# Optimization experiments

Measured on AMD Instinct MI355X. Metric: run time of the kernel, lower is better.

## Reference

```python
import jax, jax.numpy as jnp
import numpy as np
from jax import lax


def conv2d(x, w, pad):
    # NCHW / OIHW, stride 1, symmetric padding
    return lax.conv_general_dilated(x, w, (1, 1), [(pad, pad), (pad, pad)],
                                    dimension_numbers=('NCHW', 'OIHW', 'NCHW'))


def maxpool2(x):
    return lax.reduce_window(x, -jnp.inf, lax.max, (1, 1, 2, 2), (1, 1, 2, 2), 'VALID')


def batchnorm(x, g, b, eps=1e-5):
    # training-mode BN: batch statistics over (N,H,W), biased variance (matches torch)
    m = x.mean(axis=(0, 2, 3), keepdims=True)
    v = x.var(axis=(0, 2, 3), keepdims=True)
    return (x - m) * lax.rsqrt(v + eps) * g[None, :, None, None] + b[None, :, None, None]


def setup_inputs() -> dict:
    key = jax.random.key(0)
    ks = jax.random.split(key, 10)
    rn = lambda k, shape, s=0.1: jax.random.normal(k, shape, jnp.float32) * s
    return {
        'X': jax.random.normal(ks[0], (32, 3, 128, 128), jnp.float32),
        'obs': jax.random.normal(ks[1], (32, 4), jnp.float32),
        'h1_w': rn(ks[2], (64, 3, 3, 3)), 'h1_b': jnp.zeros((64,), jnp.float32),
        'bn1_g': jnp.ones((64,), jnp.float32), 'bn1_b': jnp.zeros((64,), jnp.float32),
        'h2_w': rn(ks[3], (128, 64, 3, 3)), 'h2_b': jnp.zeros((128,), jnp.float32),
        'bn2_g': jnp.ones((128,), jnp.float32), 'bn2_b': jnp.zeros((128,), jnp.float32),
        'h3_w': rn(ks[4], (128, 128, 3, 3)), 'h3_b': jnp.zeros((128,), jnp.float32),
        'bn3_g': jnp.ones((128,), jnp.float32), 'bn3_b': jnp.zeros((128,), jnp.float32),
        'r_w': rn(ks[5], (1, 128, 1, 1)),
        'q_w': rn(ks[6], (16, 1, 5, 5)),
        'w_vi': rn(ks[7], (16, 1, 5, 5)),
        'crit_w': rn(ks[8], (1, 256)), 'crit_b': jnp.zeros((1,), jnp.float32),
        'K': 40,
    }


def reference(X, obs, h1_w, h1_b, bn1_g, bn1_b, h2_w, h2_b, bn2_g, bn2_b,
              h3_w, h3_b, bn3_g, bn3_b, r_w, q_w, w_vi, crit_w, crit_b, K):
    # CNN feature extractor (obs is unused in the original forward)
    h = jax.nn.relu(batchnorm(maxpool2(conv2d(X, h1_w, 1) + h1_b[None, :, None, None]), bn1_g, bn1_b))
    h = jax.nn.relu(batchnorm(maxpool2(conv2d(h, h2_w, 1) + h2_b[None, :, None, None]), bn2_g, bn2_b))
    h = jax.nn.relu(batchnorm(maxpool2(conv2d(h, h3_w, 1) + h3_b[None, :, None, None]), bn3_g, bn3_b))
    r = conv2d(h, r_w, 0)                 # [B,1,16,16] reward map
    # conv(concat([r,v]), concat([q_w,w_vi], axis=1)) == conv(r,q_w) + conv(v,w_vi);
    # the r-branch is constant across the VI loop, so compute it once.
    conv_r = conv2d(r, q_w, 2)            # [B,l_q,16,16]
    v = conv_r.max(axis=1, keepdims=True)  # initial q = self.q(r)

    def body(i, v):
        q = conv_r + conv2d(v, w_vi, 2)
        return q.max(axis=1, keepdims=True)

    v = lax.fori_loop(0, K - 1, body, v)
    q = conv_r + conv2d(v, w_vi, 2)       # final explicit step
    v = q.max(axis=1, keepdims=True)
    critic = v.reshape(-1, 256) @ crit_w.T + crit_b  # [B,1]
    return critic, q.reshape(-1, 4096)
```

## Files before the change

kernel.cpp:

```cpp
#include <hip/hip_runtime.h>
#include <hip/hip_bf16.h>


using bf16x8 = __attribute__((ext_vector_type(8))) short;
using f32x4  = __attribute__((ext_vector_type(4))) float;

__device__ __forceinline__ unsigned short f2bf(float x) {
    union { float f; unsigned u; } v; v.f = x;
    unsigned r = (v.u + 0x7FFFu + ((v.u >> 16) & 1u)) >> 16;
    return (unsigned short)r;
}
__device__ __forceinline__ float bfhi(unsigned short h) {
    union { unsigned u; float f; } v; v.u = ((unsigned)h) << 16;
    return v.f;
}

template <int CIN>
__global__ __launch_bounds__(256)
void wt_kernel(const float* __restrict__ W, short* __restrict__ Wh,
               short* __restrict__ Wl)
{
    constexpr int TOTAL = 128 * CIN * 9;
    int i = blockIdx.x * 256 + threadIdx.x;
    if (i >= TOTAL) return;
    int ci = i & (CIN - 1);
    int j  = i / CIN;
    int tap = j % 9, co = j / 9;
    float x = W[(co * CIN + ci) * 9 + tap];
    unsigned short h = f2bf(x);
    Wh[i] = (short)h;
    Wl[i] = (short)f2bf(x - bfhi(h));
}

__global__ __launch_bounds__(256)
void conv1_pool_kernel(const float* __restrict__ X, const float* __restrict__ W,
                       const float* __restrict__ Bias, float* __restrict__ out)
{
    const int sp  = blockIdx.x;
    const int n   = blockIdx.y;
    const int ty0 = (sp >> 2) * 16;
    const int tx0 = (sp & 3) * 16;
    const int tid = threadIdx.x;
    const int px = tid & 15, py = tid >> 4;

    __shared__ float s_in[3][34][34];

    const int gy0 = 2 * ty0 - 1, gx0 = 2 * tx0 - 1;
    for (int idx = tid; idx < 3 * 1156; idx += 256) {
        int ci = idx / 1156, rem = idx - ci * 1156;
        int ly = rem / 34, lx = rem - ly * 34;
        int gy = gy0 + ly, gx = gx0 + lx;
        float v = 0.f;
        if ((unsigned)gy < 128u && (unsigned)gx < 128u)
            v = X[((n * 3 + ci) << 14) + (gy << 7) + gx];
        s_in[ci][ly][lx] = v;
    }
    __syncthreads();

    float patch[3][4][4];
    #pragma unroll
    for (int ci = 0; ci < 3; ++ci)
        #pragma unroll
        for (int r = 0; r < 4; ++r) {
            float2 a = *(const float2*)&s_in[ci][2 * py + r][2 * px];
            float2 b = *(const float2*)&s_in[ci][2 * py + r][2 * px + 2];
            patch[ci][r][0] = a.x; patch[ci][r][1] = a.y;
            patch[ci][r][2] = b.x; patch[ci][r][3] = b.y;
        }

    float* obase = out + (((size_t)(n * 64 + ty0 + py) * 64) + tx0 + px) * 64;
    #pragma unroll 1
    for (int co0 = 0; co0 < 64; co0 += 4) {
        float4 res;
        #pragma unroll
        for (int j = 0; j < 4; ++j) {
            int co = co0 + j;
            float wk[27];
            const float* wp = W + co * 27;
            #pragma unroll
            for (int k = 0; k < 27; ++k) wk[k] = wp[k];
            float b0 = Bias[co];
            float a0 = b0, a1 = b0, a2 = b0, a3 = b0;
            #pragma unroll
            for (int ci = 0; ci < 3; ++ci)
                #pragma unroll
                for (int dy = 0; dy < 3; ++dy)
                    #pragma unroll
                    for (int dx = 0; dx < 3; ++dx) {
                        float w = wk[ci * 9 + dy * 3 + dx];
                        a0 = fmaf(w, patch[ci][dy][dx],     a0);
                        a1 = fmaf(w, patch[ci][dy][dx + 1], a1);
                        a2 = fmaf(w, patch[ci][dy + 1][dx], a2);
                        a3 = fmaf(w, patch[ci][dy + 1][dx + 1], a3);
                    }
            float m = fmaxf(fmaxf(a0, a1), fmaxf(a2, a3));
            if (j == 0) res.x = m; else if (j == 1) res.y = m;
            else if (j == 2) res.z = m; else res.w = m;
        }
        *(float4*)(obase + co0) = res;
    }
}

template <int C>
__global__ __launch_bounds__(256)
void bn_partial_kernel(const float* __restrict__ data, int total,
                       float* __restrict__ partials)
{
    const int b = blockIdx.x, t = threadIdx.x;
    float s = 0.f, s2 = 0.f;
    for (int i = b * 256 + t; i < total; i += 256 * 256) {
        float v = data[i];
        s += v; s2 += v * v;
    }
    __shared__ float rs[256], rs2[256];
    rs[t] = s; rs2[t] = s2;
    __syncthreads();
    if (t < C) {
        #pragma unroll
        for (int off = C; off < 256; off += C) { s += rs[t + off]; s2 += rs2[t + off]; }
        partials[(b * C + t) * 2]     = s;
        partials[(b * C + t) * 2 + 1] = s2;
    }
}

__global__ __launch_bounds__(128)
void bn_finalize_kernel(const float* __restrict__ partials, int C, float cnt,
                        const float* __restrict__ g, const float* __restrict__ bb,
                        float* __restrict__ a_out, float* __restrict__ c_out)
{
    int t = threadIdx.x;
    if (t >= C) return;
    float s = 0.f, s2 = 0.f;
    for (int i = 0; i < 256; ++i) {
        s  += partials[(i * C + t) * 2];
        s2 += partials[(i * C + t) * 2 + 1];
    }
    float mean = s / cnt;
    float var  = s2 / cnt - mean * mean;
    float a = g[t] * rsqrtf(var + 1e-5f);
    a_out[t] = a;
    c_out[t] = bb[t] - mean * a;
}

template <int CIN, int WIN>
__global__ __launch_bounds__(256, 3)
void conv_mfma_kernel(const float* __restrict__ in, const float* __restrict__ bna,
                      const float* __restrict__ bnc, const short* __restrict__ Wth,
                      const short* __restrict__ Wtl, const float* __restrict__ Bias,
                      float* __restrict__ out)
{
    constexpr int CC    = CIN / 32;
    constexpr int POW   = WIN / 2;
    constexpr int TILES = WIN / 16;
    const int bx  = blockIdx.x;
    const int coh = blockIdx.y;
    const int n   = blockIdx.z;
    const int ty = bx / TILES, tx = bx % TILES;
    const int y0 = ty * 16, x0 = tx * 16;
    const int tid  = threadIdx.x;
    const int w    = tid >> 6;
    const int lane = tid & 63;
    const int lrow = lane & 15;
    const int seg  = lane >> 4;

    __shared__ __align__(16) short sA[2][4][324][8];

    f32x4 acc[4][4];
    #pragma unroll
    for (int mf = 0; mf < 4; ++mf)
        #pragma unroll
        for (int nf = 0; nf < 4; ++nf) acc[mf][nf] = (f32x4){0.f, 0.f, 0.f, 0.f};

    #pragma unroll 1
    for (int c = 0; c < CC; ++c) {
        #pragma unroll
        for (int rep = 0; rep < 6; ++rep) {
            int u = tid + rep * 256;
            if (u < 1296) {
                int slot = u / 324, p = u - slot * 324;
                int hy = p / 18, hx = p - hy * 18;
                int y = y0 - 1 + hy, x = x0 - 1 + hx;
                int cb = c * 32 + slot * 8;
                float4 f0 = make_float4(0.f, 0.f, 0.f, 0.f);
                float4 f1 = make_float4(0.f, 0.f, 0.f, 0.f);
                if ((unsigned)y < (unsigned)WIN && (unsigned)x < (unsigned)WIN) {
                    const float* s = in + (size_t)((n * WIN + y) * WIN + x) * CIN + cb;
                    f0 = *(const float4*)s;
                    f1 = *(const float4*)(s + 4);
                }
                float4 a0 = *(const float4*)(bna + cb);
                float4 a1 = *(const float4*)(bna + cb + 4);
                float4 c0 = *(const float4*)(bnc + cb);
                float4 c1 = *(const float4*)(bnc + cb + 4);
                float e[8] = {
                    fmaxf(fmaf(f0.x, a0.x, c0.x), 0.f),
                    fmaxf(fmaf(f0.y, a0.y, c0.y), 0.f),
                    fmaxf(fmaf(f0.z, a0.z, c0.z), 0.f),
                    fmaxf(fmaf(f0.w, a0.w, c0.w), 0.f),
                    fmaxf(fmaf(f1.x, a1.x, c1.x), 0.f),
                    fmaxf(fmaf(f1.y, a1.y, c1.y), 0.f),
                    fmaxf(fmaf(f1.z, a1.z, c1.z), 0.f),
                    fmaxf(fmaf(f1.w, a1.w, c1.w), 0.f)};
                unsigned hpk[4], lpk[4];
                #pragma unroll
                for (int q = 0; q < 4; ++q) {
                    unsigned short h0 = f2bf(e[2 * q]), h1 = f2bf(e[2 * q + 1]);
                    unsigned short l0 = f2bf(e[2 * q] - bfhi(h0));
                    unsigned short l1 = f2bf(e[2 * q + 1] - bfhi(h1));
                    hpk[q] = (unsigned)h0 | ((unsigned)h1 << 16);
                    lpk[q] = (unsigned)l0 | ((unsigned)l1 << 16);
                }
                *(int4*)&sA[0][slot][p][0] =
                    make_int4((int)hpk[0], (int)hpk[1], (int)hpk[2], (int)hpk[3]);
                *(int4*)&sA[1][slot][p][0] =
                    make_int4((int)lpk[0], (int)lpk[1], (int)lpk[2], (int)lpk[3]);
            }
        }
        __syncthreads();

        const short* baseH = &sA[0][0][0][0];
        const short* baseL = &sA[1][0][0][0];
        #pragma unroll 3
        for (int tap = 0; tap < 9; ++tap) {
            const int dy = tap / 3, dx = tap % 3;
            bf16x8 ah[4], al[4];
            #pragma unroll
            for (int mf = 0; mf < 4; ++mf) {
                int idx = seg * 324 + (w * 4 + mf + dy) * 18 + (lrow + dx);
                ah[mf] = *(const bf16x8*)(baseH + idx * 8);
                al[mf] = *(const bf16x8*)(baseL + idx * 8);
            }
            #pragma unroll
            for (int nf = 0; nf < 4; ++nf) {
                int co = coh * 64 + nf * 16 + lrow;
                const short* wp = Wth + ((size_t)(co * 9 + tap)) * CIN + c * 32 + seg * 8;
                const short* wq = Wtl + ((size_t)(co * 9 + tap)) * CIN + c * 32 + seg * 8;
                bf16x8 bh = *(const bf16x8*)wp;
                bf16x8 bl = *(const bf16x8*)wq;
                #pragma unroll
                for (int mf = 0; mf < 4; ++mf) {
                    acc[mf][nf] = __builtin_amdgcn_mfma_f32_16x16x32_bf16(
                        ah[mf], bh, acc[mf][nf], 0, 0, 0);
                    acc[mf][nf] = __builtin_amdgcn_mfma_f32_16x16x32_bf16(
                        al[mf], bh, acc[mf][nf], 0, 0, 0);
                    acc[mf][nf] = __builtin_amdgcn_mfma_f32_16x16x32_bf16(
                        ah[mf], bl, acc[mf][nf], 0, 0, 0);
                }
            }
        }
        __syncthreads();
    }

    #pragma unroll
    for (int mf = 0; mf < 4; mf += 2) {
        const int ypo = (y0 >> 1) + w * 2 + (mf >> 1);
        const int xp0 = (x0 >> 1) + seg * 2;
        #pragma unroll
        for (int nf = 0; nf < 4; ++nf) {
            int co = coh * 64 + nf * 16 + lrow;
            float bv = Bias[co];
            f32x4 u = acc[mf][nf], v = acc[mf + 1][nf];
            float o0 = fmaxf(fmaxf(u[0], u[1]), fmaxf(v[0], v[1]));
            float o1 = fmaxf(fmaxf(u[2], u[3]), fmaxf(v[2], v[3]));
            float* ob = out + (size_t)((n * POW + ypo) * POW + xp0) * 128 + co;
            ob[0]   = o0 + bv;
            ob[128] = o1 + bv;
        }
    }
}

__global__ __launch_bounds__(256)
void vin_kernel(const float* __restrict__ pool3, const float* __restrict__ bn_a,
                const float* __restrict__ bn_c, const float* __restrict__ r_w,
                const float* __restrict__ q_w, const float* __restrict__ w_vi,
                const float* __restrict__ crit_w, const float* __restrict__ crit_b,
                const int* __restrict__ Kp, float* __restrict__ out_critic,
                float* __restrict__ out_q)
{
    const int n = blockIdx.x;
    const int tid = threadIdx.x;
    const int px = tid & 15, py = tid >> 4;

    __shared__ float s_cr[16][256];
    __shared__ float s_v[20][20];
    __shared__ float s_qw[16][25];
    __shared__ float s_wvi[16][25];
    __shared__ float s_rw[128];
    __shared__ float s_red[256];

    for (int i = tid; i < 400; i += 256) {
        s_qw[i / 25][i % 25]  = q_w[i];
        s_wvi[i / 25][i % 25] = w_vi[i];
        s_v[i / 20][i % 20]   = 0.f;
    }
    if (tid < 128) s_rw[tid] = r_w[tid];
    __syncthreads();

    float r = 0.f;
    const float* p3 = pool3 + ((size_t)n * 256 + tid) * 128;
    #pragma unroll 1
    for (int ci0 = 0; ci0 < 128; ci0 += 4) {
        float4 v4 = *(const float4*)(p3 + ci0);
        float e[4] = {v4.x, v4.y, v4.z, v4.w};
        #pragma unroll
        for (int j = 0; j < 4; ++j) {
            float x = fmaxf(fmaf(e[j], bn_a[ci0 + j], bn_c[ci0 + j]), 0.f);
            r = fmaf(x, s_rw[ci0 + j], r);
        }
    }
    s_v[py + 2][px + 2] = r;
    __syncthreads();

    float cr[16];
    #pragma unroll
    for (int co = 0; co < 16; ++co) cr[co] = 0.f;
    #pragma unroll
    for (int dy = 0; dy < 5; ++dy)
        #pragma unroll
        for (int dx = 0; dx < 5; ++dx) {
            float rv = s_v[py + dy][px + dx];
            #pragma unroll
            for (int co = 0; co < 16; ++co)
                cr[co] = fmaf(s_qw[co][dy * 5 + dx], rv, cr[co]);
        }
    float v = cr[0];
    #pragma unroll
    for (int co = 0; co < 16; ++co) { s_cr[co][tid] = cr[co]; v = fmaxf(v, cr[co]); }
    __syncthreads();
    s_v[py + 2][px + 2] = v;
    __syncthreads();

    const int K = Kp[0];
    float q[16];
    #pragma unroll 1
    for (int it = 0; it < K; ++it) {
        #pragma unroll
        for (int co = 0; co < 16; ++co) q[co] = s_cr[co][tid];
        #pragma unroll
        for (int dy = 0; dy < 5; ++dy)
            #pragma unroll
            for (int dx = 0; dx < 5; ++dx) {
                float vv = s_v[py + dy][px + dx];
                #pragma unroll
                for (int co = 0; co < 16; ++co)
                    q[co] = fmaf(s_wvi[co][dy * 5 + dx], vv, q[co]);
            }
        float nv = q[0];
        #pragma unroll
        for (int co = 1; co < 16; ++co) nv = fmaxf(nv, q[co]);
        __syncthreads();
        s_v[py + 2][px + 2] = nv;
        __syncthreads();
        v = nv;
    }

    #pragma unroll
    for (int co = 0; co < 16; ++co)
        out_q[(size_t)n * 4096 + co * 256 + tid] = q[co];

    s_red[tid] = v * crit_w[tid];
    __syncthreads();
    for (int off = 128; off > 0; off >>= 1) {
        if (tid < off) s_red[tid] += s_red[tid + off];
        __syncthreads();
    }
    if (tid == 0) out_critic[n] = s_red[0] + crit_b[0];
}

extern "C" void kernel_launch(void* const* d_in, const int* in_sizes, int n_in,
                              void* d_out, int out_size, void* d_ws, size_t ws_size,
                              hipStream_t stream)
{
    const float* X      = (const float*)d_in[0];
    const float* h1_w   = (const float*)d_in[2];
    const float* h1_b   = (const float*)d_in[3];
    const float* bn1_g  = (const float*)d_in[4];
    const float* bn1_b  = (const float*)d_in[5];
    const float* h2_w   = (const float*)d_in[6];
    const float* h2_b   = (const float*)d_in[7];
    const float* bn2_g  = (const float*)d_in[8];
    const float* bn2_b  = (const float*)d_in[9];
    const float* h3_w   = (const float*)d_in[10];
    const float* h3_b   = (const float*)d_in[11];
    const float* bn3_g  = (const float*)d_in[12];
    const float* bn3_b  = (const float*)d_in[13];
    const float* r_w    = (const float*)d_in[14];
    const float* q_w    = (const float*)d_in[15];
    const float* w_vi   = (const float*)d_in[16];
    const float* crit_w = (const float*)d_in[17];
    const float* crit_b = (const float*)d_in[18];
    const int*   Kp     = (const int*)d_in[19];

    float* ws    = (float*)d_ws;
    short* W2H   = (short*)(ws);
    short* W2L   = (short*)(ws + 36864);
    short* W3H   = (short*)(ws + 73728);
    short* W3L   = (short*)(ws + 147456);
    float* part  = ws + 221184;
    float* prm   = ws + 286720;
    float* a1 = prm, *c1 = prm + 64, *a2 = prm + 128, *c2 = prm + 256,
         * a3 = prm + 384, *c3 = prm + 512;
    float* buf1  = ws + 287744;
    float* buf2  = ws + 8676352;
    float* pool3 = ws + 287744;

    float* out_critic = (float*)d_out;
    float* out_q      = out_critic + 32;

    wt_kernel<64><<<(128 * 64 * 9 + 255) / 256, 256, 0, stream>>>(h2_w, W2H, W2L);
    wt_kernel<128><<<(128 * 128 * 9 + 255) / 256, 256, 0, stream>>>(h3_w, W3H, W3L);

    conv1_pool_kernel<<<dim3(16, 32), 256, 0, stream>>>(X, h1_w, h1_b, buf1);

    bn_partial_kernel<64><<<256, 256, 0, stream>>>(buf1, 8388608, part);
    bn_finalize_kernel<<<1, 128, 0, stream>>>(part, 64, 131072.f, bn1_g, bn1_b, a1, c1);

    conv_mfma_kernel<64, 64><<<dim3(16, 2, 32), 256, 0, stream>>>(
        buf1, a1, c1, W2H, W2L, h2_b, buf2);

    bn_partial_kernel<128><<<256, 256, 0, stream>>>(buf2, 4194304, part);
    bn_finalize_kernel<<<1, 128, 0, stream>>>(part, 128, 32768.f, bn2_g, bn2_b, a2, c2);

    conv_mfma_kernel<128, 32><<<dim3(4, 2, 32), 256, 0, stream>>>(
        buf2, a2, c2, W3H, W3L, h3_b, pool3);

    bn_partial_kernel<128><<<256, 256, 0, stream>>>(pool3, 1048576, part);
    bn_finalize_kernel<<<1, 128, 0, stream>>>(part, 128, 8192.f, bn3_g, bn3_b, a3, c3);

    vin_kernel<<<32, 256, 0, stream>>>(pool3, a3, c3, r_w, q_w, w_vi,
                                       crit_w, crit_b, Kp, out_critic, out_q);
}
```

Baseline: 507.1 us.

## Prefetch next channel chunk during MFMA compute and relayout conv weights

The conv MFMA kernel now issues global loads for the next 32-channel chunk into registers before computing the current chunk, then converts and writes them to LDS afterwards. The goal is to hide global load latency behind the MFMA work. Weights are pre-permuted into a layout that makes each lane's fragment load contiguous, and BN scale/shift are staged in shared memory. Conv3 also splits output channels over four blocks (NF=2) for more parallelism. The extra prefetch registers lower the occupancy hint from 3 to 2 waves.

```diff
diff --git a/kernel.cpp b/kernel.cpp
--- a/kernel.cpp
+++ b/kernel.cpp
@@ -20,16 +20,20 @@
 void wt_kernel(const float* __restrict__ W, short* __restrict__ Wh,
                short* __restrict__ Wl)
 {
+    constexpr int CC = CIN / 32;
     constexpr int TOTAL = 128 * CIN * 9;
     int i = blockIdx.x * 256 + threadIdx.x;
     if (i >= TOTAL) return;
-    int ci = i & (CIN - 1);
+    int ci = i % CIN;
     int j  = i / CIN;
     int tap = j % 9, co = j / 9;
     float x = W[(co * CIN + ci) * 9 + tap];
+    int c = ci >> 5, seg = (ci >> 3) & 3, e = ci & 7;
+    int cb = co >> 4, lr = co & 15;
+    size_t oi = ((((size_t)(tap * CC + c) * 8 + cb) * 4 + seg) * 16 + lr) * 8 + e;
     unsigned short h = f2bf(x);
-    Wh[i] = (short)h;
-    Wl[i] = (short)f2bf(x - bfhi(h));
+    Wh[oi] = (short)h;
+    Wl[oi] = (short)f2bf(x - bfhi(h));
 }
 
 __global__ __launch_bounds__(256)
@@ -142,8 +146,8 @@
     c_out[t] = bb[t] - mean * a;
 }
 
-template <int CIN, int WIN>
-__global__ __launch_bounds__(256, 3)
+template <int CIN, int WIN, int NF>
+__global__ __launch_bounds__(256, 2)
 void conv_mfma_kernel(const float* __restrict__ in, const float* __restrict__ bna,
                       const float* __restrict__ bnc, const short* __restrict__ Wth,
                       const short* __restrict__ Wtl, const float* __restrict__ Bias,
@@ -158,106 +162,139 @@
     const int ty = bx / TILES, tx = bx % TILES;
     const int y0 = ty * 16, x0 = tx * 16;
     const int tid  = threadIdx.x;
-    const int w    = tid >> 6;
+    const int wv   = tid >> 6;
     const int lane = tid & 63;
     const int lrow = lane & 15;
     const int seg  = lane >> 4;
-
-    __shared__ __align__(16) short sA[2][4][324][8];
-
-    f32x4 acc[4][4];
+    const int cbase = coh * NF;
+
+    __shared__ __align__(16) short sAs[2 * 4 * 324 * 8];
+    __shared__ float sBnA[128], sBnC[128];
+
+    if (tid < CIN) { sBnA[tid] = bna[tid]; sBnC[tid] = bnc[tid]; }
+
+    int offs[6], lds16[6], cia[6];
+    unsigned vmask = 0;
+    #pragma unroll
+    for (int rep = 0; rep < 6; ++rep) {
+        int u = tid + rep * 256;
+        int slot = u / 324, p = u - slot * 324;
+        int hy = p / 18, hx = p - hy * 18;
+        int y = y0 - 1 + hy, x = x0 - 1 + hx;
+        bool act = (u < 1296);
+        bool val = act && ((unsigned)y < (unsigned)WIN) && ((unsigned)x < (unsigned)WIN);
+        offs[rep]  = ((n * WIN + y) * WIN + x) * CIN + slot * 8;
+        lds16[rep] = slot * 324 + p;
+        cia[rep]   = slot * 8;
+        if (val) vmask |= 1u << rep;
+    }
+
+    float4 pa[6], pb[6];
+
+#define ISSUE_LOADS(cc) \
+    _Pragma("unroll") \
+    for (int rep = 0; rep < 6; ++rep) { \
+        float4 z; z.x = 0.f; z.y = 0.f; z.z = 0.f; z.w = 0.f; \
+        pa[rep] = z; pb[rep] = z; \
+        if ((vmask >> rep) & 1u) { \
+            const float* s_ = in + offs[rep] + (cc) * 32; \
+            pa[rep] = *(const float4*)s_; \
+            pb[rep] = *(const float4*)(s_ + 4); \
+        } \
+    }
+
+#define CONVERT_WRITE(cc) \
+    _Pragma("unroll") \
+    for (int rep = 0; rep < 6; ++rep) { \
+        if (rep < 5 || tid < 16) { \
+            const float* ba_ = sBnA + (cc) * 32 + cia[rep]; \
+            const float* bc_ = sBnC + (cc) * 32 + cia[rep]; \
+            float4 a0_ = *(const float4*)ba_, a1_ = *(const float4*)(ba_ + 4); \
+            float4 c0_ = *(const float4*)bc_, c1_ = *(const float4*)(bc_ + 4); \
+            float e_[8] = { \
+                fmaxf(fmaf(pa[rep].x, a0_.x, c0_.x), 0.f), \
+                fmaxf(fmaf(pa[rep].y, a0_.y, c0_.y), 0.f), \
+                fmaxf(fmaf(pa[rep].z, a0_.z, c0_.z), 0.f), \
+                fmaxf(fmaf(pa[rep].w, a0_.w, c0_.w), 0.f), \
+                fmaxf(fmaf(pb[rep].x, a1_.x, c1_.x), 0.f), \
+                fmaxf(fmaf(pb[rep].y, a1_.y, c1_.y), 0.f), \
+                fmaxf(fmaf(pb[rep].z, a1_.z, c1_.z), 0.f), \
+                fmaxf(fmaf(pb[rep].w, a1_.w, c1_.w), 0.f)}; \
+            unsigned hpk_[4], lpk_[4]; \
+            _Pragma("unroll") \
+            for (int q = 0; q < 4; ++q) { \
+                unsigned short h0_ = f2bf(e_[2 * q]), h1_ = f2bf(e_[2 * q + 1]); \
+                unsigned short l0_ = f2bf(e_[2 * q] - bfhi(h0_)); \
+                unsigned short l1_ = f2bf(e_[2 * q + 1] - bfhi(h1_)); \
+                hpk_[q] = (unsigned)h0_ | ((unsigned)h1_ << 16); \
+                lpk_[q] = (unsigned)l0_ | ((unsigned)l1_ << 16); \
+            } \
+            *(int4*)&sAs[lds16[rep] * 8] = \
+                make_int4((int)hpk_[0], (int)hpk_[1], (int)hpk_[2], (int)hpk_[3]); \
+            *(int4*)&sAs[10368 + lds16[rep] * 8] = \
+                make_int4((int)lpk_[0], (int)lpk_[1], (int)lpk_[2], (int)lpk_[3]); \
+        } \
+    }
+
+#define COMPUTE(cc) \
+    { const short* baseH_ = sAs; const short* baseL_ = sAs + 10368; \
+      _Pragma("unroll 3") \
+      for (int tap = 0; tap < 9; ++tap) { \
+          const int dy_ = tap / 3, dx_ = tap % 3; \
+          bf16x8 ah_[4], al_[4]; \
+          _Pragma("unroll") \
+          for (int mf = 0; mf < 4; ++mf) { \
+              int idx_ = seg * 324 + (wv * 4 + mf + dy_) * 18 + (lrow + dx_); \
+              ah_[mf] = *(const bf16x8*)(baseH_ + idx_ * 8); \
+              al_[mf] = *(const bf16x8*)(baseL_ + idx_ * 8); \
+          } \
+          _Pragma("unroll") \
+          for (int nf = 0; nf < NF; ++nf) { \
+              size_t wo_ = ((((size_t)(tap * CC + (cc)) * 8 + cbase + nf) * 4 + seg) * 16 + lrow) * 8; \
+              bf16x8 bh_ = *(const bf16x8*)(Wth + wo_); \
+              bf16x8 bl_ = *(const bf16x8*)(Wtl + wo_); \
+              _Pragma("unroll") \
+              for (int mf = 0; mf < 4; ++mf) { \
+                  acc[mf][nf] = __builtin_amdgcn_mfma_f32_16x16x32_bf16(ah_[mf], bh_, acc[mf][nf], 0, 0, 0); \
+                  acc[mf][nf] = __builtin_amdgcn_mfma_f32_16x16x32_bf16(al_[mf], bh_, acc[mf][nf], 0, 0, 0); \
+                  acc[mf][nf] = __builtin_amdgcn_mfma_f32_16x16x32_bf16(ah_[mf], bl_, acc[mf][nf], 0, 0, 0); \
+              } \
+          } \
+      } }
+
+    f32x4 acc[4][NF];
     #pragma unroll
     for (int mf = 0; mf < 4; ++mf)
         #pragma unroll
-        for (int nf = 0; nf < 4; ++nf) acc[mf][nf] = (f32x4){0.f, 0.f, 0.f, 0.f};
+        for (int nf = 0; nf < NF; ++nf) acc[mf][nf] = (f32x4){0.f, 0.f, 0.f, 0.f};
+
+    ISSUE_LOADS(0)
+    __syncthreads();
+    CONVERT_WRITE(0)
+    __syncthreads();
 
     #pragma unroll 1
     for (int c = 0; c < CC; ++c) {
-        #pragma unroll
-        for (int rep = 0; rep < 6; ++rep) {
-            int u = tid + rep * 256;
-            if (u < 1296) {
-                int slot = u / 324, p = u - slot * 324;
-                int hy = p / 18, hx = p - hy * 18;
-                int y = y0 - 1 + hy, x = x0 - 1 + hx;
-                int cb = c * 32 + slot * 8;
-                float4 f0 = make_float4(0.f, 0.f, 0.f, 0.f);
-                float4 f1 = make_float4(0.f, 0.f, 0.f, 0.f);
-                if ((unsigned)y < (unsigned)WIN && (unsigned)x < (unsigned)WIN) {
-                    const float* s = in + (size_t)((n * WIN + y) * WIN + x) * CIN + cb;
-                    f0 = *(const float4*)s;
-                    f1 = *(const float4*)(s + 4);
-                }
-                float4 a0 = *(const float4*)(bna + cb);
-                float4 a1 = *(const float4*)(bna + cb + 4);
-                float4 c0 = *(const float4*)(bnc + cb);
-                float4 c1 = *(const float4*)(bnc + cb + 4);
-                float e[8] = {
-                    fmaxf(fmaf(f0.x, a0.x, c0.x), 0.f),
-                    fmaxf(fmaf(f0.y, a0.y, c0.y), 0.f),
-                    fmaxf(fmaf(f0.z, a0.z, c0.z), 0.f),
-                    fmaxf(fmaf(f0.w, a0.w, c0.w), 0.f),
-                    fmaxf(fmaf(f1.x, a1.x, c1.x), 0.f),
-                    fmaxf(fmaf(f1.y, a1.y, c1.y), 0.f),
-                    fmaxf(fmaf(f1.z, a1.z, c1.z), 0.f),
-                    fmaxf(fmaf(f1.w, a1.w, c1.w), 0.f)};
-                unsigned hpk[4], lpk[4];
-                #pragma unroll
-                for (int q = 0; q < 4; ++q) {
-                    unsigned short h0 = f2bf(e[2 * q]), h1 = f2bf(e[2 * q + 1]);
-                    unsigned short l0 = f2bf(e[2 * q] - bfhi(h0));
-                    unsigned short l1 = f2bf(e[2 * q + 1] - bfhi(h1));
-                    hpk[q] = (unsigned)h0 | ((unsigned)h1 << 16);
-                    lpk[q] = (unsigned)l0 | ((unsigned)l1 << 16);
-                }
-                *(int4*)&sA[0][slot][p][0] =
-                    make_int4((int)hpk[0], (int)hpk[1], (int)hpk[2], (int)hpk[3]);
-                *(int4*)&sA[1][slot][p][0] =
-                    make_int4((int)lpk[0], (int)lpk[1], (int)lpk[2], (int)lpk[3]);
-            }
-        }
+        if (c + 1 < CC) ISSUE_LOADS(c + 1)
+        COMPUTE(c)
         __syncthreads();
-
-        const short* baseH = &sA[0][0][0][0];
-        const short* baseL = &sA[1][0][0][0];
-        #pragma unroll 3
-        for (int tap = 0; tap < 9; ++tap) {
-            const int dy = tap / 3, dx = tap % 3;
-            bf16x8 ah[4], al[4];
-            #pragma unroll
-            for (int mf = 0; mf < 4; ++mf) {
-                int idx = seg * 324 + (w * 4 + mf + dy) * 18 + (lrow + dx);
-                ah[mf] = *(const bf16x8*)(baseH + idx * 8);
-                al[mf] = *(const bf16x8*)(baseL + idx * 8);
-            }
-            #pragma unroll
-            for (int nf = 0; nf < 4; ++nf) {
-                int co = coh * 64 + nf * 16 + lrow;
-                const short* wp = Wth + ((size_t)(co * 9 + tap)) * CIN + c * 32 + seg * 8;
-                const short* wq = Wtl + ((size_t)(co * 9 + tap)) * CIN + c * 32 + seg * 8;
-                bf16x8 bh = *(const bf16x8*)wp;
-                bf16x8 bl = *(const bf16x8*)wq;
-                #pragma unroll
-                for (int mf = 0; mf < 4; ++mf) {
-                    acc[mf][nf] = __builtin_amdgcn_mfma_f32_16x16x32_bf16(
-                        ah[mf], bh, acc[mf][nf], 0, 0, 0);
-                    acc[mf][nf] = __builtin_amdgcn_mfma_f32_16x16x32_bf16(
-                        al[mf], bh, acc[mf][nf], 0, 0, 0);
-                    acc[mf][nf] = __builtin_amdgcn_mfma_f32_16x16x32_bf16(
-                        ah[mf], bl, acc[mf][nf], 0, 0, 0);
-                }
-            }
-        }
-        __syncthreads();
-    }
+        if (c + 1 < CC) {
+            CONVERT_WRITE(c + 1)
+            __syncthreads();
+        }
+    }
+
+#undef ISSUE_LOADS
+#undef CONVERT_WRITE
+#undef COMPUTE
 
     #pragma unroll
     for (int mf = 0; mf < 4; mf += 2) {
-        const int ypo = (y0 >> 1) + w * 2 + (mf >> 1);
+        const int ypo = (y0 >> 1) + wv * 2 + (mf >> 1);
         const int xp0 = (x0 >> 1) + seg * 2;
         #pragma unroll
-        for (int nf = 0; nf < 4; ++nf) {
-            int co = coh * 64 + nf * 16 + lrow;
+        for (int nf = 0; nf < NF; ++nf) {
+            int co = (cbase + nf) * 16 + lrow;
             float bv = Bias[co];
             f32x4 u = acc[mf][nf], v = acc[mf + 1][nf];
             float o0 = fmaxf(fmaxf(u[0], u[1]), fmaxf(v[0], v[1]));
@@ -415,13 +452,13 @@
     bn_partial_kernel<64><<<256, 256, 0, stream>>>(buf1, 8388608, part);
     bn_finalize_kernel<<<1, 128, 0, stream>>>(part, 64, 131072.f, bn1_g, bn1_b, a1, c1);
 
-    conv_mfma_kernel<64, 64><<<dim3(16, 2, 32), 256, 0, stream>>>(
+    conv_mfma_kernel<64, 64, 4><<<dim3(16, 2, 32), 256, 0, stream>>>(
         buf1, a1, c1, W2H, W2L, h2_b, buf2);
 
     bn_partial_kernel<128><<<256, 256, 0, stream>>>(buf2, 4194304, part);
     bn_finalize_kernel<<<1, 128, 0, stream>>>(part, 128, 32768.f, bn2_g, bn2_b, a2, c2);
 
-    conv_mfma_kernel<128, 32><<<dim3(4, 2, 32), 256, 0, stream>>>(
+    conv_mfma_kernel<128, 32, 2><<<dim3(4, 4, 32), 256, 0, stream>>>(
         buf2, a2, c2, W3H, W3L, h3_b, pool3);
 
     bn_partial_kernel<128><<<256, 256, 0, stream>>>(pool3, 1048576, part);
```

New measurement: 431.4 us. 1.18x faster.
